# Kernel tuning notes

Measured on AMD Instinct MI355X. Metric: run time of the kernel, lower is better.

The kernel has to match this reference:

```python
import jax, jax.numpy as jnp
import numpy as np

SEQ_LEN = 2_097_152  # free sequence dimension
NUM_SYMBOLS = 10
NUM_STATES = 10
NUM_CLASSES = 2


def setup_inputs() -> dict:
    key = jax.random.key(0)
    k1, k2, k3, k4 = jax.random.split(key, 4)
    # x[t] is a probability distribution over symbols (soft one-hot), matching
    # the automaton semantics and keeping the 2M-step recurrence numerically stable.
    x = jax.random.uniform(k1, (SEQ_LEN, NUM_SYMBOLS), dtype=jnp.float32)
    x = x / jnp.sum(x, axis=1, keepdims=True)
    # Parameters, initialized exactly as in the torch module (__init__ softmaxes).
    P = jax.nn.softmax(jax.random.normal(k2, (NUM_SYMBOLS, NUM_STATES, NUM_STATES), dtype=jnp.float32), axis=2)
    start_state = jax.nn.softmax(jax.random.normal(k3, (NUM_STATES,), dtype=jnp.float32), axis=0)
    accept_states = jax.nn.softmax(jax.random.normal(k4, (NUM_STATES, NUM_CLASSES), dtype=jnp.float32), axis=1)
    return {"x": x, "P": P, "start_state": start_state, "accept_states": accept_states}


def reference(x, P, start_state, accept_states):
    # Sequential recurrence: s_{t+1} = s_t @ (sum_k x[t,k] * P[k])
    def step(s, xt):
        Wt = jnp.einsum('k,kij->ij', xt, P)  # [S, S] symbol-weighted transition
        return s @ Wt, None
    s, _ = jax.lax.scan(step, start_state, x)
    return s @ accept_states  # [num_classes]
```

## Files before the change

kernel.cpp:

```cpp
#include <hip/hip_runtime.h>

#define TEN 10


__device__ __forceinline__ void tree64(float* lds, int tid)
{
    const int q     = tid >> 2;
    const int sub   = tid & 3;
    const int rbase = (sub == 3) ? 8 : sub * 3;
    const int r0 = rbase, r1 = rbase + 1;
    const int r2 = (rbase + 2 > 9) ? 9 : rbase + 2;
    const bool w2 = (sub < 2);

    for (int np = 32; np >= 1; np >>= 1) {
        float c[3][TEN];
        if (q < np) {
            const float* A = lds + (2 * q) * 120;
            const float* B = lds + (2 * q + 1) * 120;
            float ar[3][TEN];
#pragma unroll
            for (int t = 0; t < 3; ++t) {
                const int rt = (t == 0) ? r0 : (t == 1) ? r1 : r2;
                const float4 a0 = reinterpret_cast<const float4*>(A + rt * 12)[0];
                const float4 a1 = reinterpret_cast<const float4*>(A + rt * 12)[1];
                const float2 a2 = reinterpret_cast<const float2*>(A + rt * 12 + 8)[0];
                ar[t][0]=a0.x; ar[t][1]=a0.y; ar[t][2]=a0.z; ar[t][3]=a0.w;
                ar[t][4]=a1.x; ar[t][5]=a1.y; ar[t][6]=a1.z; ar[t][7]=a1.w;
                ar[t][8]=a2.x; ar[t][9]=a2.y;
#pragma unroll
                for (int j = 0; j < TEN; ++j) c[t][j] = 0.0f;
            }
#pragma unroll
            for (int a = 0; a < TEN; ++a) {
                const float4 b0 = reinterpret_cast<const float4*>(B + a * 12)[0];
                const float4 b1 = reinterpret_cast<const float4*>(B + a * 12)[1];
                const float2 b2 = reinterpret_cast<const float2*>(B + a * 12 + 8)[0];
#pragma unroll
                for (int t = 0; t < 3; ++t) {
                    const float ma = ar[t][a];
                    c[t][0] = fmaf(ma, b0.x, c[t][0]);
                    c[t][1] = fmaf(ma, b0.y, c[t][1]);
                    c[t][2] = fmaf(ma, b0.z, c[t][2]);
                    c[t][3] = fmaf(ma, b0.w, c[t][3]);
                    c[t][4] = fmaf(ma, b1.x, c[t][4]);
                    c[t][5] = fmaf(ma, b1.y, c[t][5]);
                    c[t][6] = fmaf(ma, b1.z, c[t][6]);
                    c[t][7] = fmaf(ma, b1.w, c[t][7]);
                    c[t][8] = fmaf(ma, b2.x, c[t][8]);
                    c[t][9] = fmaf(ma, b2.y, c[t][9]);
                }
            }
        }
        __syncthreads();
        if (q < np) {
            float* C = lds + q * 120;
#pragma unroll
            for (int t = 0; t < 3; ++t) {
                const int rt = (t == 0) ? r0 : (t == 1) ? r1 : r2;
                if (t < 2 || w2) {
                    float* cr = C + rt * 12;
                    reinterpret_cast<float4*>(cr)[0] = make_float4(c[t][0], c[t][1], c[t][2], c[t][3]);
                    reinterpret_cast<float4*>(cr)[1] = make_float4(c[t][4], c[t][5], c[t][6], c[t][7]);
                    reinterpret_cast<float2*>(cr + 8)[0] = make_float2(c[t][8], c[t][9]);
                }
            }
        }
        __syncthreads();
    }
}

__global__ __attribute__((amdgpu_flat_work_group_size(256, 256),
                          amdgpu_waves_per_eu(1, 1)))
void automaton_chunks(const float* __restrict__ x, const float* __restrict__ P,
                      float* __restrict__ outBlk, int L)
{
    __shared__ __align__(16) float lds[8448];

    const int tid  = threadIdx.x;
    const int wave = tid >> 6;
    const int lane = tid & 63;
    const int cl   = lane >> 2;
    const int sub  = lane & 3;
    const int cib  = wave * 16 + cl;
    const long long chunk = (long long)blockIdx.x * 64 + cib;

    const int rbase = (sub == 3) ? 8 : sub * 3;
    const int r0 = rbase, r1 = rbase + 1;
    const int r2 = (rbase + 2 > 9) ? 9 : rbase + 2;
    const bool w2 = (sub < 2);

    float p[3][TEN][TEN];
    {
        const int rr[3] = {r0, r1, r2};
#pragma unroll
        for (int t = 0; t < 3; ++t)
#pragma unroll
            for (int k = 0; k < TEN; ++k) {
                const float2* pp = reinterpret_cast<const float2*>(P + k * 100 + rr[t] * TEN);
                const float2 a0 = pp[0], a1 = pp[1], a2 = pp[2], a3 = pp[3], a4 = pp[4];
                p[t][k][0]=a0.x; p[t][k][1]=a0.y; p[t][k][2]=a1.x; p[t][k][3]=a1.y;
                p[t][k][4]=a2.x; p[t][k][5]=a2.y; p[t][k][6]=a3.x; p[t][k][7]=a3.y;
                p[t][k][8]=a4.x; p[t][k][9]=a4.y;
            }
    }

    float m[3][TEN];
#pragma unroll
    for (int t = 0; t < 3; ++t) {
        const int rt = (t == 0) ? r0 : (t == 1) ? r1 : r2;
#pragma unroll
        for (int j = 0; j < TEN; ++j) m[t][j] = (j == rt) ? 1.0f : 0.0f;
    }

    float* wc = lds + cib * 132;
    const float2* xp = reinterpret_cast<const float2*>(x) + (size_t)chunk * L * 5;

    float2 nx0 = xp[0], nx1 = xp[1], nx2 = xp[2], nx3 = xp[3], nx4 = xp[4];
    xp += 5;

#pragma unroll 1
    for (int s = 0; s < L; ++s) {
        const float xv[TEN] = {nx0.x, nx0.y, nx1.x, nx1.y, nx2.x,
                               nx2.y, nx3.x, nx3.y, nx4.x, nx4.y};
        if (s + 1 < L) {
            nx0 = xp[0]; nx1 = xp[1]; nx2 = xp[2]; nx3 = xp[3]; nx4 = xp[4];
            xp += 5;
        }

#pragma unroll
        for (int t = 0; t < 3; ++t) {
            float w[TEN];
#pragma unroll
            for (int j = 0; j < TEN; ++j) {
                float acc = xv[0] * p[t][0][j];
#pragma unroll
                for (int k = 1; k < TEN; ++k) acc = fmaf(xv[k], p[t][k][j], acc);
                w[j] = acc;
            }
            const int rt = (t == 0) ? r0 : (t == 1) ? r1 : r2;
            if (t < 2 || w2) {
                float* wr = wc + rt * 12;
                reinterpret_cast<float4*>(wr)[0] = make_float4(w[0], w[1], w[2], w[3]);
                reinterpret_cast<float4*>(wr)[1] = make_float4(w[4], w[5], w[6], w[7]);
                reinterpret_cast<float2*>(wr + 8)[0] = make_float2(w[8], w[9]);
            }
        }
        __builtin_amdgcn_wave_barrier();

        float mn[3][TEN];
#pragma unroll
        for (int t = 0; t < 3; ++t)
#pragma unroll
            for (int j = 0; j < TEN; ++j) mn[t][j] = 0.0f;

#pragma unroll
        for (int a = 0; a < TEN; ++a) {
            const float4 b0 = reinterpret_cast<const float4*>(wc + a * 12)[0];
            const float4 b1 = reinterpret_cast<const float4*>(wc + a * 12)[1];
            const float2 b2 = reinterpret_cast<const float2*>(wc + a * 12 + 8)[0];
#pragma unroll
            for (int t = 0; t < 3; ++t) {
                const float ma = m[t][a];
                mn[t][0] = fmaf(ma, b0.x, mn[t][0]);
                mn[t][1] = fmaf(ma, b0.y, mn[t][1]);
                mn[t][2] = fmaf(ma, b0.z, mn[t][2]);
                mn[t][3] = fmaf(ma, b0.w, mn[t][3]);
                mn[t][4] = fmaf(ma, b1.x, mn[t][4]);
                mn[t][5] = fmaf(ma, b1.y, mn[t][5]);
                mn[t][6] = fmaf(ma, b1.z, mn[t][6]);
                mn[t][7] = fmaf(ma, b1.w, mn[t][7]);
                mn[t][8] = fmaf(ma, b2.x, mn[t][8]);
                mn[t][9] = fmaf(ma, b2.y, mn[t][9]);
            }
        }
#pragma unroll
        for (int t = 0; t < 3; ++t)
#pragma unroll
            for (int j = 0; j < TEN; ++j) m[t][j] = mn[t][j];
        __builtin_amdgcn_wave_barrier();
    }

    __syncthreads();
    {
        float* dst = lds + cib * 120;
#pragma unroll
        for (int t = 0; t < 3; ++t) {
            const int rt = (t == 0) ? r0 : (t == 1) ? r1 : r2;
            if (t < 2 || w2) {
                float* dr = dst + rt * 12;
                reinterpret_cast<float4*>(dr)[0] = make_float4(m[t][0], m[t][1], m[t][2], m[t][3]);
                reinterpret_cast<float4*>(dr)[1] = make_float4(m[t][4], m[t][5], m[t][6], m[t][7]);
                reinterpret_cast<float2*>(dr + 8)[0] = make_float2(m[t][8], m[t][9]);
            }
        }
    }
    __syncthreads();
    tree64(lds, tid);

    if (tid < 4) {
        const int sb = tid;
        const int rb = (sb == 3) ? 8 : sb * 3;
#pragma unroll
        for (int t = 0; t < 3; ++t) {
            const int rt = (t == 0) ? rb : (t == 1) ? rb + 1 : ((rb + 2 > 9) ? 9 : rb + 2);
            if (t < 2 || sb < 2) {
                const float* src = lds + rt * 12;
                float* dr = outBlk + (size_t)blockIdx.x * 100 + rt * TEN;
#pragma unroll
                for (int j = 0; j < TEN; ++j) dr[j] = src[j];
            }
        }
    }
}

__global__ void automaton_final(const float* __restrict__ blkM,
                                const float* __restrict__ start,
                                const float* __restrict__ acc,
                                float* __restrict__ outv)
{
    __shared__ __align__(16) float lds[7680];
    __shared__ float sv[TEN];
    const int tid = threadIdx.x;
    const int q   = tid >> 2;
    const int sub = tid & 3;
    const int rbase = (sub == 3) ? 8 : sub * 3;
    const int r0 = rbase, r1 = rbase + 1;
    const int r2 = (rbase + 2 > 9) ? 9 : rbase + 2;
    const bool w2 = (sub < 2);
    const int rr0 = r0, rr1 = r1, rr2 = r2;

    float a[3][TEN];
    {
        const int rr[3] = {rr0, rr1, rr2};
        const float* A0 = blkM + (size_t)(4 * q) * 100;
#pragma unroll
        for (int t = 0; t < 3; ++t) {
            const float2* pp = reinterpret_cast<const float2*>(A0 + rr[t] * TEN);
            const float2 a0 = pp[0], a1 = pp[1], a2 = pp[2], a3 = pp[3], a4 = pp[4];
            a[t][0]=a0.x; a[t][1]=a0.y; a[t][2]=a1.x; a[t][3]=a1.y; a[t][4]=a2.x;
            a[t][5]=a2.y; a[t][6]=a3.x; a[t][7]=a3.y; a[t][8]=a4.x; a[t][9]=a4.y;
        }
    }
#pragma unroll 1
    for (int i = 1; i < 4; ++i) {
        const float* B = blkM + (size_t)(4 * q + i) * 100;
        float c[3][TEN];
#pragma unroll
        for (int t = 0; t < 3; ++t)
#pragma unroll
            for (int j = 0; j < TEN; ++j) c[t][j] = 0.0f;
#pragma unroll
        for (int aa = 0; aa < TEN; ++aa) {
            const float2* br = reinterpret_cast<const float2*>(B + aa * TEN);
            const float2 b0 = br[0], b1 = br[1], b2 = br[2], b3 = br[3], b4 = br[4];
#pragma unroll
            for (int t = 0; t < 3; ++t) {
                const float ma = a[t][aa];
                c[t][0] = fmaf(ma, b0.x, c[t][0]);
                c[t][1] = fmaf(ma, b0.y, c[t][1]);
                c[t][2] = fmaf(ma, b1.x, c[t][2]);
                c[t][3] = fmaf(ma, b1.y, c[t][3]);
                c[t][4] = fmaf(ma, b2.x, c[t][4]);
                c[t][5] = fmaf(ma, b2.y, c[t][5]);
                c[t][6] = fmaf(ma, b3.x, c[t][6]);
                c[t][7] = fmaf(ma, b3.y, c[t][7]);
                c[t][8] = fmaf(ma, b4.x, c[t][8]);
                c[t][9] = fmaf(ma, b4.y, c[t][9]);
            }
        }
#pragma unroll
        for (int t = 0; t < 3; ++t)
#pragma unroll
            for (int j = 0; j < TEN; ++j) a[t][j] = c[t][j];
    }
    {
        float* dst = lds + q * 120;
#pragma unroll
        for (int t = 0; t < 3; ++t) {
            const int rt = (t == 0) ? rr0 : (t == 1) ? rr1 : rr2;
            if (t < 2 || w2) {
                float* dr = dst + rt * 12;
                reinterpret_cast<float4*>(dr)[0] = make_float4(a[t][0], a[t][1], a[t][2], a[t][3]);
                reinterpret_cast<float4*>(dr)[1] = make_float4(a[t][4], a[t][5], a[t][6], a[t][7]);
                reinterpret_cast<float2*>(dr + 8)[0] = make_float2(a[t][8], a[t][9]);
            }
        }
    }
    __syncthreads();
    tree64(lds, tid);

    if (tid < TEN) {
        const int j = tid;
        float v = 0.0f;
#pragma unroll
        for (int r = 0; r < TEN; ++r) v = fmaf(start[r], lds[r * 12 + j], v);
        sv[j] = v;
    }
    __syncthreads();
    if (tid == 0) {
        float o0 = 0.0f, o1 = 0.0f;
#pragma unroll
        for (int j = 0; j < TEN; ++j) {
            o0 = fmaf(sv[j], acc[2 * j + 0], o0);
            o1 = fmaf(sv[j], acc[2 * j + 1], o1);
        }
        outv[0] = o0;
        outv[1] = o1;
    }
}

extern "C" void kernel_launch(void* const* d_in, const int* in_sizes, int n_in,
                              void* d_out, int out_size, void* d_ws, size_t ws_size,
                              hipStream_t stream)
{
    const float* x     = (const float*)d_in[0];
    const float* P     = (const float*)d_in[1];
    const float* start = (const float*)d_in[2];
    const float* acc   = (const float*)d_in[3];
    float* out         = (float*)d_out;

    const long long T = (long long)in_sizes[0] / TEN;
    const int L = (int)(T / 16384);

    float* blkM = (float*)d_ws;

    automaton_chunks<<<256, 256, 0, stream>>>(x, P, blkM, L);
    automaton_final<<<1, 256, 0, stream>>>(blkM, start, acc, out);
}
```

Measured before the change: 311.0 us.

## Split each chunk across five lanes by column pairs, 48 chunks per block

Reworks the chunk kernel so each chunk's 10x10 product is handled by 5 lanes, each owning two columns, instead of 4 lanes owning up to three rows. Each lane now builds its two W columns in registers and shares M through LDS, so there is less per-lane register state and less redundant W work. The total chunk count drops to 12288 (48 per block, with uneven chunk lengths computed from T), which leaves 4 idle lanes per wave. The in-block reduction becomes a ping-pong tree over 48 matrices with one thread per row. This changes the per-step serial length, lane utilisation and register pressure, and the uneven chunk split adds some imbalance.

```diff
diff --git a/kernel.cpp b/kernel.cpp
--- a/kernel.cpp
+++ b/kernel.cpp
@@ -2,6 +2,180 @@
 
 #define TEN 10
 
+__global__ __attribute__((amdgpu_flat_work_group_size(256, 256),
+                          amdgpu_waves_per_eu(1, 1)))
+void automaton_chunks(const float* __restrict__ x, const float* __restrict__ P,
+                      float* __restrict__ outBlk, long long T, int C)
+{
+    __shared__ __align__(16) float lds[8704];
+
+    const int tid  = threadIdx.x;
+    const int wave = tid >> 6;
+    const int lane = tid & 63;
+    const int grp  = lane / 5;
+    const int sub  = lane % 5;
+    const bool active = (grp < 12);
+    const int cib  = wave * 12 + grp;
+    const int j0 = 2 * sub, j1 = j0 + 1;
+
+    float p[2][TEN][TEN];
+    float m[TEN][2];
+    long long Lc = 0;
+    const float2* xp = nullptr;
+    float* slot = lds + (active ? cib : 0) * 132;
+
+    if (active) {
+        const long long chunk = (long long)blockIdx.x * 48 + cib;
+        const long long s0 = chunk * T / C;
+        const long long s1 = (chunk + 1) * T / C;
+        Lc = s1 - s0;
+        xp = reinterpret_cast<const float2*>(x) + s0 * 5;
+#pragma unroll
+        for (int k = 0; k < TEN; ++k)
+#pragma unroll
+            for (int a = 0; a < TEN; ++a) {
+                const float2 v = *reinterpret_cast<const float2*>(P + k * 100 + a * TEN + j0);
+                p[0][k][a] = v.x;
+                p[1][k][a] = v.y;
+            }
+#pragma unroll
+        for (int r = 0; r < TEN; ++r) {
+            m[r][0] = (r == j0) ? 1.0f : 0.0f;
+            m[r][1] = (r == j1) ? 1.0f : 0.0f;
+        }
+    }
+
+    float2 nx0, nx1, nx2, nx3, nx4;
+    if (active) { nx0 = xp[0]; nx1 = xp[1]; nx2 = xp[2]; nx3 = xp[3]; nx4 = xp[4]; xp += 5; }
+
+    if (active) {
+#pragma unroll 1
+        for (long long s = 0; s < Lc; ++s) {
+            const float xv[TEN] = {nx0.x, nx0.y, nx1.x, nx1.y, nx2.x,
+                                   nx2.y, nx3.x, nx3.y, nx4.x, nx4.y};
+            if (s + 1 < Lc) {
+                nx0 = xp[0]; nx1 = xp[1]; nx2 = xp[2]; nx3 = xp[3]; nx4 = xp[4];
+                xp += 5;
+            }
+
+            {
+                float* c0 = slot + j0 * 12;
+                reinterpret_cast<float4*>(c0)[0] = make_float4(m[0][0], m[1][0], m[2][0], m[3][0]);
+                reinterpret_cast<float4*>(c0)[1] = make_float4(m[4][0], m[5][0], m[6][0], m[7][0]);
+                reinterpret_cast<float2*>(c0 + 8)[0] = make_float2(m[8][0], m[9][0]);
+                float* c1 = slot + j1 * 12;
+                reinterpret_cast<float4*>(c1)[0] = make_float4(m[0][1], m[1][1], m[2][1], m[3][1]);
+                reinterpret_cast<float4*>(c1)[1] = make_float4(m[4][1], m[5][1], m[6][1], m[7][1]);
+                reinterpret_cast<float2*>(c1 + 8)[0] = make_float2(m[8][1], m[9][1]);
+            }
+            __builtin_amdgcn_wave_barrier();
+
+            float w0[TEN], w1[TEN];
+#pragma unroll
+            for (int a = 0; a < TEN; ++a) {
+                float a0 = xv[0] * p[0][0][a];
+                float a1 = xv[0] * p[1][0][a];
+#pragma unroll
+                for (int k = 1; k < TEN; ++k) {
+                    a0 = fmaf(xv[k], p[0][k][a], a0);
+                    a1 = fmaf(xv[k], p[1][k][a], a1);
+                }
+                w0[a] = a0; w1[a] = a1;
+            }
+
+            float mn[TEN][2];
+#pragma unroll
+            for (int r = 0; r < TEN; ++r) { mn[r][0] = 0.0f; mn[r][1] = 0.0f; }
+#pragma unroll
+            for (int a = 0; a < TEN; ++a) {
+                const float4 v0 = reinterpret_cast<const float4*>(slot + a * 12)[0];
+                const float4 v1 = reinterpret_cast<const float4*>(slot + a * 12)[1];
+                const float2 v2 = reinterpret_cast<const float2*>(slot + a * 12 + 8)[0];
+                const float ca[TEN] = {v0.x, v0.y, v0.z, v0.w, v1.x, v1.y, v1.z, v1.w, v2.x, v2.y};
+                const float wa0 = w0[a], wa1 = w1[a];
+#pragma unroll
+                for (int r = 0; r < TEN; ++r) {
+                    mn[r][0] = fmaf(ca[r], wa0, mn[r][0]);
+                    mn[r][1] = fmaf(ca[r], wa1, mn[r][1]);
+                }
+            }
+#pragma unroll
+            for (int r = 0; r < TEN; ++r) { m[r][0] = mn[r][0]; m[r][1] = mn[r][1]; }
+            __builtin_amdgcn_wave_barrier();
+        }
+    }
+
+    __syncthreads();
+    if (active) {
+        float* t = lds + cib * 120;
+#pragma unroll
+        for (int r = 0; r < TEN; ++r) {
+            t[r * 12 + j0] = m[r][0];
+            t[r * 12 + j1] = m[r][1];
+        }
+    }
+    __syncthreads();
+
+    {
+        const float* src = lds;
+        float* dst = lds + 5760;
+        int n = 48;
+        while (n > 3) {
+            const int np = n >> 1;
+            const int pI = tid / TEN;
+            const int r  = tid % TEN;
+            if (pI < np) {
+                const float* A = src + (2 * pI) * 120;
+                const float* B = src + (2 * pI + 1) * 120;
+                float ar[TEN];
+#pragma unroll
+                for (int j = 0; j < TEN; ++j) ar[j] = A[r * 12 + j];
+                float c[TEN] = {0, 0, 0, 0, 0, 0, 0, 0, 0, 0};
+#pragma unroll
+                for (int a = 0; a < TEN; ++a) {
+                    const float ma = ar[a];
+#pragma unroll
+                    for (int j = 0; j < TEN; ++j) c[j] = fmaf(ma, B[a * 12 + j], c[j]);
+                }
+                float* C = dst + pI * 120;
+#pragma unroll
+                for (int j = 0; j < TEN; ++j) C[r * 12 + j] = c[j];
+            }
+            __syncthreads();
+            const float* ts = src; src = dst; dst = const_cast<float*>(ts);
+            n = np;
+        }
+        if (tid < TEN) {
+            const int r = tid;
+            float ar[TEN];
+#pragma unroll
+            for (int j = 0; j < TEN; ++j) ar[j] = src[r * 12 + j];
+            float c[TEN] = {0, 0, 0, 0, 0, 0, 0, 0, 0, 0};
+#pragma unroll
+            for (int a = 0; a < TEN; ++a) {
+                const float ma = ar[a];
+#pragma unroll
+                for (int j = 0; j < TEN; ++j) c[j] = fmaf(ma, src[120 + a * 12 + j], c[j]);
+            }
+#pragma unroll
+            for (int j = 0; j < TEN; ++j) lds[5760 + r * 12 + j] = c[j];
+        }
+        __syncthreads();
+        if (tid < TEN) {
+            const int r = tid;
+            float c[TEN] = {0, 0, 0, 0, 0, 0, 0, 0, 0, 0};
+#pragma unroll
+            for (int a = 0; a < TEN; ++a) {
+                const float ma = lds[5760 + r * 12 + a];
+#pragma unroll
+                for (int j = 0; j < TEN; ++j) c[j] = fmaf(ma, src[240 + a * 12 + j], c[j]);
+            }
+            float* dr = outBlk + (size_t)blockIdx.x * 100 + r * TEN;
+#pragma unroll
+            for (int j = 0; j < TEN; ++j) dr[j] = c[j];
+        }
+    }
+}
 
 __device__ __forceinline__ void tree64(float* lds, int tid)
 {
@@ -35,19 +209,12 @@
                 const float4 b0 = reinterpret_cast<const float4*>(B + a * 12)[0];
                 const float4 b1 = reinterpret_cast<const float4*>(B + a * 12)[1];
                 const float2 b2 = reinterpret_cast<const float2*>(B + a * 12 + 8)[0];
+                const float br[TEN] = {b0.x,b0.y,b0.z,b0.w,b1.x,b1.y,b1.z,b1.w,b2.x,b2.y};
 #pragma unroll
                 for (int t = 0; t < 3; ++t) {
                     const float ma = ar[t][a];
-                    c[t][0] = fmaf(ma, b0.x, c[t][0]);
-                    c[t][1] = fmaf(ma, b0.y, c[t][1]);
-                    c[t][2] = fmaf(ma, b0.z, c[t][2]);
-                    c[t][3] = fmaf(ma, b0.w, c[t][3]);
-                    c[t][4] = fmaf(ma, b1.x, c[t][4]);
-                    c[t][5] = fmaf(ma, b1.y, c[t][5]);
-                    c[t][6] = fmaf(ma, b1.z, c[t][6]);
-                    c[t][7] = fmaf(ma, b1.w, c[t][7]);
-                    c[t][8] = fmaf(ma, b2.x, c[t][8]);
-                    c[t][9] = fmaf(ma, b2.y, c[t][9]);
+#pragma unroll
+                    for (int j = 0; j < TEN; ++j) c[t][j] = fmaf(ma, br[j], c[t][j]);
                 }
             }
         }
@@ -66,150 +233,6 @@
             }
         }
         __syncthreads();
-    }
-}
-
-__global__ __attribute__((amdgpu_flat_work_group_size(256, 256),
-                          amdgpu_waves_per_eu(1, 1)))
-void automaton_chunks(const float* __restrict__ x, const float* __restrict__ P,
-                      float* __restrict__ outBlk, int L)
-{
-    __shared__ __align__(16) float lds[8448];
-
-    const int tid  = threadIdx.x;
-    const int wave = tid >> 6;
-    const int lane = tid & 63;
-    const int cl   = lane >> 2;
-    const int sub  = lane & 3;
-    const int cib  = wave * 16 + cl;
-    const long long chunk = (long long)blockIdx.x * 64 + cib;
-
-    const int rbase = (sub == 3) ? 8 : sub * 3;
-    const int r0 = rbase, r1 = rbase + 1;
-    const int r2 = (rbase + 2 > 9) ? 9 : rbase + 2;
-    const bool w2 = (sub < 2);
-
-    float p[3][TEN][TEN];
-    {
-        const int rr[3] = {r0, r1, r2};
-#pragma unroll
-        for (int t = 0; t < 3; ++t)
-#pragma unroll
-            for (int k = 0; k < TEN; ++k) {
-                const float2* pp = reinterpret_cast<const float2*>(P + k * 100 + rr[t] * TEN);
-                const float2 a0 = pp[0], a1 = pp[1], a2 = pp[2], a3 = pp[3], a4 = pp[4];
-                p[t][k][0]=a0.x; p[t][k][1]=a0.y; p[t][k][2]=a1.x; p[t][k][3]=a1.y;
-                p[t][k][4]=a2.x; p[t][k][5]=a2.y; p[t][k][6]=a3.x; p[t][k][7]=a3.y;
-                p[t][k][8]=a4.x; p[t][k][9]=a4.y;
-            }
-    }
-
-    float m[3][TEN];
-#pragma unroll
-    for (int t = 0; t < 3; ++t) {
-        const int rt = (t == 0) ? r0 : (t == 1) ? r1 : r2;
-#pragma unroll
-        for (int j = 0; j < TEN; ++j) m[t][j] = (j == rt) ? 1.0f : 0.0f;
-    }
-
-    float* wc = lds + cib * 132;
-    const float2* xp = reinterpret_cast<const float2*>(x) + (size_t)chunk * L * 5;
-
-    float2 nx0 = xp[0], nx1 = xp[1], nx2 = xp[2], nx3 = xp[3], nx4 = xp[4];
-    xp += 5;
-
-#pragma unroll 1
-    for (int s = 0; s < L; ++s) {
-        const float xv[TEN] = {nx0.x, nx0.y, nx1.x, nx1.y, nx2.x,
-                               nx2.y, nx3.x, nx3.y, nx4.x, nx4.y};
-        if (s + 1 < L) {
-            nx0 = xp[0]; nx1 = xp[1]; nx2 = xp[2]; nx3 = xp[3]; nx4 = xp[4];
-            xp += 5;
-        }
-
-#pragma unroll
-        for (int t = 0; t < 3; ++t) {
-            float w[TEN];
-#pragma unroll
-            for (int j = 0; j < TEN; ++j) {
-                float acc = xv[0] * p[t][0][j];
-#pragma unroll
-                for (int k = 1; k < TEN; ++k) acc = fmaf(xv[k], p[t][k][j], acc);
-                w[j] = acc;
-            }
-            const int rt = (t == 0) ? r0 : (t == 1) ? r1 : r2;
-            if (t < 2 || w2) {
-                float* wr = wc + rt * 12;
-                reinterpret_cast<float4*>(wr)[0] = make_float4(w[0], w[1], w[2], w[3]);
-                reinterpret_cast<float4*>(wr)[1] = make_float4(w[4], w[5], w[6], w[7]);
-                reinterpret_cast<float2*>(wr + 8)[0] = make_float2(w[8], w[9]);
-            }
-        }
-        __builtin_amdgcn_wave_barrier();
-
-        float mn[3][TEN];
-#pragma unroll
-        for (int t = 0; t < 3; ++t)
-#pragma unroll
-            for (int j = 0; j < TEN; ++j) mn[t][j] = 0.0f;
-
-#pragma unroll
-        for (int a = 0; a < TEN; ++a) {
-            const float4 b0 = reinterpret_cast<const float4*>(wc + a * 12)[0];
-            const float4 b1 = reinterpret_cast<const float4*>(wc + a * 12)[1];
-            const float2 b2 = reinterpret_cast<const float2*>(wc + a * 12 + 8)[0];
-#pragma unroll
-            for (int t = 0; t < 3; ++t) {
-                const float ma = m[t][a];
-                mn[t][0] = fmaf(ma, b0.x, mn[t][0]);
-                mn[t][1] = fmaf(ma, b0.y, mn[t][1]);
-                mn[t][2] = fmaf(ma, b0.z, mn[t][2]);
-                mn[t][3] = fmaf(ma, b0.w, mn[t][3]);
-                mn[t][4] = fmaf(ma, b1.x, mn[t][4]);
-                mn[t][5] = fmaf(ma, b1.y, mn[t][5]);
-                mn[t][6] = fmaf(ma, b1.z, mn[t][6]);
-                mn[t][7] = fmaf(ma, b1.w, mn[t][7]);
-                mn[t][8] = fmaf(ma, b2.x, mn[t][8]);
-                mn[t][9] = fmaf(ma, b2.y, mn[t][9]);
-            }
-        }
-#pragma unroll
-        for (int t = 0; t < 3; ++t)
-#pragma unroll
-            for (int j = 0; j < TEN; ++j) m[t][j] = mn[t][j];
-        __builtin_amdgcn_wave_barrier();
-    }
-
-    __syncthreads();
-    {
-        float* dst = lds + cib * 120;
-#pragma unroll
-        for (int t = 0; t < 3; ++t) {
-            const int rt = (t == 0) ? r0 : (t == 1) ? r1 : r2;
-            if (t < 2 || w2) {
-                float* dr = dst + rt * 12;
-                reinterpret_cast<float4*>(dr)[0] = make_float4(m[t][0], m[t][1], m[t][2], m[t][3]);
-                reinterpret_cast<float4*>(dr)[1] = make_float4(m[t][4], m[t][5], m[t][6], m[t][7]);
-                reinterpret_cast<float2*>(dr + 8)[0] = make_float2(m[t][8], m[t][9]);
-            }
-        }
-    }
-    __syncthreads();
-    tree64(lds, tid);
-
-    if (tid < 4) {
-        const int sb = tid;
-        const int rb = (sb == 3) ? 8 : sb * 3;
-#pragma unroll
-        for (int t = 0; t < 3; ++t) {
-            const int rt = (t == 0) ? rb : (t == 1) ? rb + 1 : ((rb + 2 > 9) ? 9 : rb + 2);
-            if (t < 2 || sb < 2) {
-                const float* src = lds + rt * 12;
-                float* dr = outBlk + (size_t)blockIdx.x * 100 + rt * TEN;
-#pragma unroll
-                for (int j = 0; j < TEN; ++j) dr[j] = src[j];
-            }
-        }
     }
 }
 
@@ -224,10 +247,9 @@
     const int q   = tid >> 2;
     const int sub = tid & 3;
     const int rbase = (sub == 3) ? 8 : sub * 3;
-    const int r0 = rbase, r1 = rbase + 1;
-    const int r2 = (rbase + 2 > 9) ? 9 : rbase + 2;
+    const int rr0 = rbase, rr1 = rbase + 1;
+    const int rr2 = (rbase + 2 > 9) ? 9 : rbase + 2;
     const bool w2 = (sub < 2);
-    const int rr0 = r0, rr1 = r1, rr2 = r2;
 
     float a[3][TEN];
     {
@@ -253,19 +275,12 @@
         for (int aa = 0; aa < TEN; ++aa) {
             const float2* br = reinterpret_cast<const float2*>(B + aa * TEN);
             const float2 b0 = br[0], b1 = br[1], b2 = br[2], b3 = br[3], b4 = br[4];
+            const float bv[TEN] = {b0.x,b0.y,b1.x,b1.y,b2.x,b2.y,b3.x,b3.y,b4.x,b4.y};
 #pragma unroll
             for (int t = 0; t < 3; ++t) {
                 const float ma = a[t][aa];
-                c[t][0] = fmaf(ma, b0.x, c[t][0]);
-                c[t][1] = fmaf(ma, b0.y, c[t][1]);
-                c[t][2] = fmaf(ma, b1.x, c[t][2]);
-                c[t][3] = fmaf(ma, b1.y, c[t][3]);
-                c[t][4] = fmaf(ma, b2.x, c[t][4]);
-                c[t][5] = fmaf(ma, b2.y, c[t][5]);
-                c[t][6] = fmaf(ma, b3.x, c[t][6]);
-                c[t][7] = fmaf(ma, b3.y, c[t][7]);
-                c[t][8] = fmaf(ma, b4.x, c[t][8]);
-                c[t][9] = fmaf(ma, b4.y, c[t][9]);
+#pragma unroll
+                for (int j = 0; j < TEN; ++j) c[t][j] = fmaf(ma, bv[j], c[t][j]);
             }
         }
 #pragma unroll
@@ -320,10 +335,10 @@
     float* out         = (float*)d_out;
 
     const long long T = (long long)in_sizes[0] / TEN;
-    const int L = (int)(T / 16384);
+    const int C = 12288;
 
     float* blkM = (float*)d_ws;
 
-    automaton_chunks<<<256, 256, 0, stream>>>(x, P, blkM, L);
+    automaton_chunks<<<256, 256, 0, stream>>>(x, P, blkM, T, C);
     automaton_final<<<1, 256, 0, stream>>>(blkM, start, acc, out);
 }
```

Result: faster. 266.7 us (-14.2%).
